# Kernel tuning notes

Measured on AMD Instinct MI355X. Metric: run time of the kernel, lower is better.

The kernel has to match this reference:

```python
import jax, jax.numpy as jnp
import numpy as np

L, B, E, H = 2048, 2, 1024, 16
HD = E // H


def setup_inputs() -> dict:
    key = jax.random.key(0)
    ks = jax.random.split(key, 5)
    s = 0.02
    return {
        "query": jax.random.normal(ks[0], (L, B, E), jnp.float32),
        "key": jax.random.normal(ks[1], (L, B, E), jnp.float32),
        "value": jax.random.normal(ks[2], (L, B, E), jnp.float32),
        "in_proj_weight": jax.random.normal(ks[3], (3 * E, E), jnp.float32) * s,
        "in_proj_bias": jnp.zeros((3 * E,), jnp.float32),
        "out_proj_weight": jax.random.normal(ks[4], (E, E), jnp.float32) * s,
        "out_proj_bias": jnp.zeros((E,), jnp.float32),
    }


def reference(query, key, value, in_proj_weight, in_proj_bias, out_proj_weight, out_proj_bias):
    # torch nn.MultiheadAttention math, seq-first [L, B, E], causal mask
    # (attend_mode='only_attend_front': positions j > i are masked).
    w_q, w_k, w_v = jnp.split(in_proj_weight, 3, axis=0)
    b_q, b_k, b_v = jnpp_split(in_proj_bias) if False else jnp.split(in_proj_bias, 3, axis=0)
    q = query @ w_q.T + b_q            # [L, B, E]
    k = key @ w_k.T + b_k
    v = value @ w_v.T + b_v

    def heads(x):  # [L, B, E] -> [B, H, L, HD]
        return x.reshape(x.shape[0], x.shape[1], H, HD).transpose(1, 2, 0, 3)

    qh, kh, vh = heads(q), heads(k), heads(v)
    scale = 1.0 / jnp.sqrt(jnp.asarray(HD, q.dtype))
    scores = jnp.einsum("bhqd,bhkd->bhqk", qh * scale, kh)  # [B, H, L, L]
    causal = jnp.triu(jnp.ones((scores.shape[-2], scores.shape[-1]), bool), k=1)
    scores = jnp.where(causal, jnp.asarray(-jnp.inf, scores.dtype), scores)
    attn = jax.nn.softmax(scores, axis=-1)
    out = jnp.einsum("bhqk,bhkd->bhqd", attn, vh)           # [B, H, L, HD]
    out = out.transpose(2, 0, 1, 3).reshape(query.shape[0], query.shape[1], E)  # [L, B, E]
    out = out @ out_proj_weight.T + out_proj_bias
    # torch also returns head-averaged attn weights [B, L, L]
    attn_avg = attn.mean(axis=1)
    return out, attn_avg
```

## Files before the change

### kernel.cpp

```cpp
#include <hip/hip_runtime.h>

#define L_ 2048
#define B_ 2
#define E_ 1024
#define H_ 16
#define HD_ 64
#define M_ 4096
#define K_ 1024

typedef unsigned short u16;
typedef unsigned int u32;
using short8  = __attribute__((ext_vector_type(8))) short;
using short4v = __attribute__((ext_vector_type(4))) short;
using floatx4 = __attribute__((ext_vector_type(4))) float;

__device__ inline u16 f2b(float f) {
  unsigned u = __float_as_uint(f);
  u += 0x7FFF + ((u >> 16) & 1);
  return (u16)(u >> 16);
}

__device__ inline u32 pack2(float a, float b) {
  u32 ua = __float_as_uint(a) + 0x8000u;
  u32 ub = __float_as_uint(b) + 0x8000u;
  return (ua >> 16) | (ub & 0xFFFF0000u);
}

__device__ inline floatx4 mfma16(short8 a, short8 b, floatx4 c) {
  return __builtin_amdgcn_mfma_f32_16x16x32_bf16(a, b, c, 0, 0, 0);
}

__device__ inline void gload16(const void* g, void* l) {
  __builtin_amdgcn_global_load_lds(
      (const __attribute__((address_space(1))) u32*)g,
      (__attribute__((address_space(3))) u32*)l, 16, 0, 0);
}

__global__ void convk(const float* __restrict__ src, u16* __restrict__ dst, int n4) {
  int i = blockIdx.x * blockDim.x + threadIdx.x;
  if (i < n4) {
    float4 v = ((const float4*)src)[i];
    ushort4 o;
    o.x = f2b(v.x); o.y = f2b(v.y); o.z = f2b(v.z); o.w = f2b(v.w);
    ((ushort4*)dst)[i] = o;
  }
}

template <int MODE>
__global__ __launch_bounds__(256) void gemm128(
    const u16* __restrict__ A, const u16* __restrict__ W, const float* __restrict__ bias,
    u16* __restrict__ qh, u16* __restrict__ kh, u16* __restrict__ vhT,
    float* __restrict__ outp)
{
  __shared__ __align__(16) u16 As[128 * 32];
  __shared__ __align__(16) u16 Bs[128 * 32];
  const int p = (MODE == 0) ? blockIdx.z : 0;
  const u16* Ap = A + (size_t)p * M_ * K_;
  const u16* Wp = W + (size_t)p * E_ * K_;
  const float* bp = bias + p * E_;
  const int row0 = blockIdx.y * 128, col0 = blockIdx.x * 128;
  const int t = threadIdx.x, lane = t & 63, wv = t >> 6;
  const int lanem = lane & 15, quad = lane >> 4;
  const int wm = wv >> 1, wn = wv & 1;

  int f0 = t, f1 = 256 + t;
  int r0s = f0 >> 2, q0s = (f0 & 3) ^ ((r0s >> 1) & 3);
  int r1s = f1 >> 2, q1s = (f1 & 3) ^ ((r1s >> 1) & 3);

  floatx4 acc[4][4];
#pragma unroll
  for (int mi = 0; mi < 4; ++mi)
#pragma unroll
    for (int ni = 0; ni < 4; ++ni) acc[mi][ni] = (floatx4){0.f, 0.f, 0.f, 0.f};

  const int swz = (lanem >> 1) & 3;

  for (int k0 = 0; k0 < K_; k0 += 32) {
    __syncthreads();
    gload16(Ap + (size_t)(row0 + r0s) * K_ + k0 + q0s * 8, (char*)As + wv * 1024);
    gload16(Wp + (size_t)(col0 + r0s) * K_ + k0 + q0s * 8, (char*)Bs + wv * 1024);
    gload16(Ap + (size_t)(row0 + r1s) * K_ + k0 + q1s * 8, (char*)As + 4096 + wv * 1024);
    gload16(Wp + (size_t)(col0 + r1s) * K_ + k0 + q1s * 8, (char*)Bs + 4096 + wv * 1024);
    __syncthreads();
    short8 af[4], bfg[4];
#pragma unroll
    for (int mi = 0; mi < 4; ++mi) {
      int r = wm * 64 + mi * 16 + lanem;
      af[mi] = *(const short8*)((const char*)As + r * 64 + (quad ^ swz) * 16);
    }
#pragma unroll
    for (int ni = 0; ni < 4; ++ni) {
      int r = wn * 64 + ni * 16 + lanem;
      bfg[ni] = *(const short8*)((const char*)Bs + r * 64 + (quad ^ swz) * 16);
    }
#pragma unroll
    for (int mi = 0; mi < 4; ++mi)
#pragma unroll
      for (int ni = 0; ni < 4; ++ni)
        acc[mi][ni] = mfma16(af[mi], bfg[ni], acc[mi][ni]);
  }

#pragma unroll
  for (int ni = 0; ni < 4; ++ni) {
    int gc = col0 + wn * 64 + ni * 16 + lanem;
    float bv = bp[gc];
#pragma unroll
    for (int mi = 0; mi < 4; ++mi) {
      int gr0 = row0 + wm * 64 + mi * 16 + quad * 4;
#pragma unroll
      for (int v = 0; v < 4; ++v) {
        float val = acc[mi][ni][v] + bv;
        int r = gr0 + v;
        if (MODE == 1) {
          outp[(size_t)r * E_ + gc] = val;
        } else {
          int l = r >> 1, bb = r & 1, hh = gc >> 6, d = gc & 63;
          u16 x = f2b(val);
          if (p == 0)      qh[(((size_t)bb * H_ + hh) * L_ + l) * HD_ + d] = x;
          else if (p == 1) kh[(((size_t)bb * H_ + hh) * L_ + l) * HD_ + d] = x;
          else {
            int lp = (l & ~31) | (((l >> 2) & 3) * 8 + ((l >> 4) & 1) * 4 + (l & 3));
            vhT[(((size_t)bb * H_ + hh) * HD_ + d) * L_ + lp] = x;
          }
        }
      }
    }
  }
}

__global__ __launch_bounds__(256, 2) void attn1(
    const u16* __restrict__ qh, const u16* __restrict__ kh, const u16* __restrict__ vhT,
    u16* __restrict__ ctx, float* __restrict__ li_ws)
{
  __shared__ __align__(16) u16 Ks[2][64 * 64];
  __shared__ __align__(16) u16 Vs[2][64 * 64];
  const int g = blockIdx.x;
  const int h = blockIdx.y, b = blockIdx.z;
  const int t = threadIdx.x, lane = t & 63, wv = t >> 6;
  const int lanem = lane & 15, quad = lane >> 4;
  const int bh = b * H_ + h;
  const int gB = (L_ / 64 - 1) - g;
  const int rowA = g * 64 + wv * 16 + lanem;
  const int rowB = gB * 64 + wv * 16 + lanem;

  const u16* qpA = qh + ((size_t)bh * L_ + rowA) * HD_;
  const u16* qpB = qh + ((size_t)bh * L_ + rowB) * HD_;
  short8 qA0 = *(const short8*)(qpA + quad * 8);
  short8 qA1 = *(const short8*)(qpA + 32 + quad * 8);
  short8 qB0 = *(const short8*)(qpB + quad * 8);
  short8 qB1 = *(const short8*)(qpB + 32 + quad * 8);

  const int srow = lane >> 3;
  const int spiece = (lane & 7) ^ srow;
  const u16* ksrc = kh + ((size_t)bh * L_ + wv * 16 + srow) * HD_ + spiece * 8;
  const u16* vsrc = vhT + ((size_t)bh * HD_ + wv * 16 + srow) * L_ + spiece * 8;

  const int ntiles = 32 - g;
  auto stage = [&](int buf) {
    gload16(ksrc, (char*)Ks[buf] + wv * 2048);
    gload16(ksrc + 8 * HD_, (char*)Ks[buf] + wv * 2048 + 1024);
    gload16(vsrc, (char*)Vs[buf] + wv * 2048);
    gload16(vsrc + (size_t)8 * L_, (char*)Vs[buf] + wv * 2048 + 1024);
    ksrc += 64 * HD_;
    vsrc += 64;
  };

  const int swz = lanem & 7;
  const int cb0 = lanem * 128 + ((quad ^ swz)) * 16;
  const int cb1 = lanem * 128 + ((quad ^ swz) ^ 4) * 16;

  float liA = 0.f, liB = 0.f;
  floatx4 oA[4], oB[4];
#pragma unroll
  for (int d = 0; d < 4; ++d) { oA[d] = (floatx4){0.f,0.f,0.f,0.f}; oB[d] = oA[d]; }

  int j0 = 0, tcur = 0;

  auto do_tile = [&](int modeA, int modeB) {
    __syncthreads();
    if (tcur + 1 < ntiles) stage((tcur + 1) & 1);
    const char* kbuf = (const char*)Ks[tcur & 1];
    const char* vbuf = (const char*)Vs[tcur & 1];

    floatx4 sA[4], sB[4];
#pragma unroll
    for (int jf = 0; jf < 4; ++jf) {
      short8 a0 = *(const short8*)(kbuf + cb0 + jf * 2048);
      short8 a1 = *(const short8*)(kbuf + cb1 + jf * 2048);
      floatx4 z = (floatx4){0.f,0.f,0.f,0.f};
      if (modeA != 2) sA[jf] = mfma16(a1, qA1, mfma16(a0, qA0, z));
      sB[jf] = mfma16(a1, qB1, mfma16(a0, qB0, z));
    }

    short8 pbA[2], pbB[2];
    auto soft = [&](floatx4* st, int row, float& li, short8* pb, int masked) {
#pragma unroll
      for (int jc = 0; jc < 2; ++jc) {
        float p[8];
#pragma unroll
        for (int r = 0; r < 4; ++r) {
          int ja = j0 + jc * 32 + quad * 4 + r;
          float e0 = __expf(st[jc * 2][r] * 0.125f);
          float e1 = __expf(st[jc * 2 + 1][r] * 0.125f);
          if (masked) {
            e0 = (ja <= row) ? e0 : 0.f;
            e1 = (ja + 16 <= row) ? e1 : 0.f;
          }
          li += e0 + e1;
          p[r] = e0; p[4 + r] = e1;
        }
        union { u32 w[4]; short8 s; } u;
        u.w[0] = pack2(p[0], p[1]); u.w[1] = pack2(p[2], p[3]);
        u.w[2] = pack2(p[4], p[5]); u.w[3] = pack2(p[6], p[7]);
        pb[jc] = u.s;
      }
    };
    if (modeA == 0) soft(sA, rowA, liA, pbA, 0);
    else if (modeA == 1) soft(sA, rowA, liA, pbA, 1);
    if (modeB == 0) soft(sB, rowB, liB, pbB, 0);
    else soft(sB, rowB, liB, pbB, 1);

#pragma unroll
    for (int jc = 0; jc < 2; ++jc) {
      const int base = (jc == 0) ? cb0 : cb1;
#pragma unroll
      for (int dbl = 0; dbl < 4; ++dbl) {
        short8 vf = *(const short8*)(vbuf + base + dbl * 2048);
        if (modeA != 2) oA[dbl] = mfma16(vf, pbA[jc], oA[dbl]);
        oB[dbl] = mfma16(vf, pbB[jc], oB[dbl]);
      }
    }
    j0 += 64;
    ++tcur;
  };

  stage(0);
  for (int jt = 0; jt < g; ++jt) do_tile(0, 0);
  do_tile(1, 0);
  for (int jt = g + 1; jt <= 30 - g; ++jt) do_tile(2, 0);
  do_tile(2, 1);

  liA += __shfl_xor(liA, 16); liA += __shfl_xor(liA, 32);
  liB += __shfl_xor(liB, 16); liB += __shfl_xor(liB, 32);
  float invA = 1.0f / liA, invB = 1.0f / liB;

  u16* cA = ctx + ((size_t)rowA * B_ + b) * E_ + h * HD_ + quad * 4;
  u16* cB = ctx + ((size_t)rowB * B_ + b) * E_ + h * HD_ + quad * 4;
#pragma unroll
  for (int dbl = 0; dbl < 4; ++dbl) {
    ushort4 pkA, pkB;
    pkA.x = f2b(oA[dbl][0] * invA); pkA.y = f2b(oA[dbl][1] * invA);
    pkA.z = f2b(oA[dbl][2] * invA); pkA.w = f2b(oA[dbl][3] * invA);
    pkB.x = f2b(oB[dbl][0] * invB); pkB.y = f2b(oB[dbl][1] * invB);
    pkB.z = f2b(oB[dbl][2] * invB); pkB.w = f2b(oB[dbl][3] * invB);
    *(ushort4*)(cA + dbl * 16) = pkA;
    *(ushort4*)(cB + dbl * 16) = pkB;
  }
  if (quad == 0) {
    li_ws[(size_t)bh * L_ + rowA] = invA;
    li_ws[(size_t)bh * L_ + rowB] = invB;
  }
}

__global__ __launch_bounds__(256) void attn2(
    const u16* __restrict__ qh, const u16* __restrict__ kh,
    const float* __restrict__ li_ws, float* __restrict__ out2)
{
  __shared__ __align__(16) u16 Ks[2][2][64 * 64];
  const int jt = blockIdx.x, it = blockIdx.y, b = blockIdx.z;
  const int t = threadIdx.x, lane = t & 63, wv = t >> 6;
  const int lanem = lane & 15, quad = lane >> 4;
  const int i0 = it * 64 + wv * 16;
  const int j0 = jt * 64;
  float* ob = out2 + (size_t)b * L_ * L_;

  if (jt > it) {
    float4 z = {0.f, 0.f, 0.f, 0.f};
    float* rp = ob + (size_t)(i0 + lanem) * L_ + j0 + quad * 16;
    ((float4*)rp)[0] = z; ((float4*)rp)[1] = z;
    ((float4*)rp)[2] = z; ((float4*)rp)[3] = z;
    return;
  }

  const int srow = lane >> 3;
  const int spiece = (lane & 7) ^ srow;
  const int swz = lanem & 7;

  auto stage = [&](int p, int buf) {
#pragma unroll
    for (int hh = 0; hh < 2; ++hh) {
      const u16* kg = kh + ((size_t)(b * H_ + 2 * p + hh) * L_ + j0) * HD_;
#pragma unroll
      for (int k = wv * 2; k < wv * 2 + 2; ++k)
        gload16(kg + (size_t)(k * 8 + srow) * HD_ + spiece * 8,
                (char*)Ks[buf][hh] + k * 1024);
    }
  };
  auto loadQ = [&](int p, short8 q[2][2], floatx4 lf[2]) {
#pragma unroll
    for (int hh = 0; hh < 2; ++hh) {
      int bh = b * H_ + 2 * p + hh;
      const u16* qb = qh + ((size_t)bh * L_ + i0 + lanem) * HD_;
      q[hh][0] = *(const short8*)(qb + quad * 8);
      q[hh][1] = *(const short8*)(qb + 32 + quad * 8);
      lf[hh] = *(const floatx4*)(li_ws + (size_t)bh * L_ + i0 + quad * 4);
    }
  };

  float acc[4][4] = {};
  short8 qc[2][2]; floatx4 lc[2];
  stage(0, 0);
  loadQ(0, qc, lc);

#pragma unroll
  for (int p = 0; p < 8; ++p) {
    const int buf = p & 1;
    __syncthreads();
    if (p < 7) stage(p + 1, 1 - buf);
    short8 qn[2][2]; floatx4 ln[2];
    loadQ(p < 7 ? p + 1 : 7, qn, ln);
#pragma unroll
    for (int hh = 0; hh < 2; ++hh) {
      const char* tb = (const char*)Ks[buf][hh];
#pragma unroll
      for (int s = 0; s < 4; ++s) {
        if (j0 + s * 16 > i0 + 15) continue;
        const char* kr = tb + (s * 16 + lanem) * 128;
        short8 b0 = *(const short8*)(kr + (quad ^ swz) * 16);
        short8 b1 = *(const short8*)(kr + ((4 + quad) ^ swz) * 16);
        floatx4 sv = (floatx4){0.f, 0.f, 0.f, 0.f};
        sv = mfma16(qc[hh][0], b0, sv);
        sv = mfma16(qc[hh][1], b1, sv);
        if (j0 + s * 16 + 15 <= i0) {
#pragma unroll
          for (int r = 0; r < 4; ++r)
            acc[s][r] += __expf(sv[r] * 0.125f) * lc[hh][r];
        } else {
#pragma unroll
          for (int r = 0; r < 4; ++r) {
            int irow = i0 + quad * 4 + r;
            int jc = j0 + s * 16 + lanem;
            if (jc <= irow) acc[s][r] += __expf(sv[r] * 0.125f) * lc[hh][r];
          }
        }
      }
    }
#pragma unroll
    for (int hh = 0; hh < 2; ++hh) {
      qc[hh][0] = qn[hh][0]; qc[hh][1] = qn[hh][1]; lc[hh] = ln[hh];
    }
  }

#pragma unroll
  for (int s = 0; s < 4; ++s)
#pragma unroll
    for (int r = 0; r < 4; ++r) {
      int irow = i0 + quad * 4 + r;
      int jc = j0 + s * 16 + lanem;
      ob[(size_t)irow * L_ + jc] = acc[s][r] * (1.0f / H_);
    }
}

extern "C" void kernel_launch(void* const* d_in, const int* in_sizes, int n_in,
                              void* d_out, int out_size, void* d_ws, size_t ws_size,
                              hipStream_t stream) {
  const float* query = (const float*)d_in[0];
  const float* key   = (const float*)d_in[1];
  const float* value = (const float*)d_in[2];
  const float* w_in  = (const float*)d_in[3];
  const float* b_in  = (const float*)d_in[4];
  const float* w_out = (const float*)d_in[5];
  const float* b_out = (const float*)d_in[6];

  char* ws = (char*)d_ws;
  size_t off = 0;
  auto alloc = [&](size_t bytes) -> void* {
    void* p = ws + off;
    off += (bytes + 255) & ~(size_t)255;
    return p;
  };
  u16* w_in_b  = (u16*)alloc((size_t)3 * E_ * K_ * 2);
  u16* w_out_b = (u16*)alloc((size_t)E_ * K_ * 2);
  u16* x_b     = (u16*)alloc((size_t)3 * M_ * K_ * 2);
  u16* qh      = (u16*)alloc((size_t)B_ * H_ * L_ * HD_ * 2);
  u16* kh      = (u16*)alloc((size_t)B_ * H_ * L_ * HD_ * 2);
  u16* vhT     = (u16*)alloc((size_t)B_ * H_ * L_ * HD_ * 2);
  u16* ctx     = (u16*)alloc((size_t)M_ * E_ * 2);
  float* li_ws = (float*)alloc((size_t)B_ * H_ * L_ * 4);

  convk<<<4096, 256, 0, stream>>>(query, x_b + (size_t)0 * M_ * K_, M_ * K_ / 4);
  convk<<<4096, 256, 0, stream>>>(key,   x_b + (size_t)1 * M_ * K_, M_ * K_ / 4);
  convk<<<4096, 256, 0, stream>>>(value, x_b + (size_t)2 * M_ * K_, M_ * K_ / 4);
  convk<<<3072, 256, 0, stream>>>(w_in,  w_in_b,  3 * E_ * K_ / 4);
  convk<<<1024, 256, 0, stream>>>(w_out, w_out_b, E_ * K_ / 4);

  gemm128<0><<<dim3(E_ / 128, M_ / 128, 3), 256, 0, stream>>>(
      x_b, w_in_b, b_in, qh, kh, vhT, nullptr);

  attn1<<<dim3(L_ / 128, H_, B_), 256, 0, stream>>>(qh, kh, vhT, ctx, li_ws);

  attn2<<<dim3(L_ / 64, L_ / 64, B_), 256, 0, stream>>>(
      qh, kh, li_ws, (float*)d_out + (size_t)M_ * E_);

  gemm128<1><<<dim3(E_ / 128, M_ / 128, 1), 256, 0, stream>>>(
      ctx, w_out_b, b_out, nullptr, nullptr, nullptr, (float*)d_out);
}
```

Measured before the change: 274.3 us.

## Double-buffer GEMM LDS tiles and merge conversion launches into one kernel

The GEMM kernel now uses two LDS buffers and issues the global-to-LDS load for the next K slice before computing on the current one. This removes one barrier per iteration and aims to overlap memory latency with MFMA work. The five separate fp32-to-bf16 conversion launches are merged into a single launch indexed by blockIdx.z, which cuts launch overhead. The cost is doubled LDS use per block, which may lower occupancy, and the overlap depends on how the compiler places its memory-count waits.

```diff
diff --git a/kernel.cpp b/kernel.cpp
--- a/kernel.cpp
+++ b/kernel.cpp
@@ -36,12 +36,24 @@
       (__attribute__((address_space(3))) u32*)l, 16, 0, 0);
 }
 
-__global__ void convk(const float* __restrict__ src, u16* __restrict__ dst, int n4) {
+__global__ void convall(const float* __restrict__ q, const float* __restrict__ k,
+                        const float* __restrict__ v, const float* __restrict__ wi,
+                        const float* __restrict__ wo,
+                        u16* __restrict__ xb, u16* __restrict__ wib,
+                        u16* __restrict__ wob) {
+  const int z = blockIdx.z;
+  const float* src;
+  u16* dst;
+  int n4;
+  if (z < 3)      { src = (z == 0 ? q : (z == 1 ? k : v));
+                    dst = xb + (size_t)z * M_ * K_; n4 = M_ * K_ / 4; }
+  else if (z == 3){ src = wi; dst = wib; n4 = 3 * E_ * K_ / 4; }
+  else            { src = wo; dst = wob; n4 = E_ * K_ / 4; }
   int i = blockIdx.x * blockDim.x + threadIdx.x;
   if (i < n4) {
-    float4 v = ((const float4*)src)[i];
+    float4 val = ((const float4*)src)[i];
     ushort4 o;
-    o.x = f2b(v.x); o.y = f2b(v.y); o.z = f2b(v.z); o.w = f2b(v.w);
+    o.x = f2b(val.x); o.y = f2b(val.y); o.z = f2b(val.z); o.w = f2b(val.w);
     ((ushort4*)dst)[i] = o;
   }
 }
@@ -52,8 +64,8 @@
     u16* __restrict__ qh, u16* __restrict__ kh, u16* __restrict__ vhT,
     float* __restrict__ outp)
 {
-  __shared__ __align__(16) u16 As[128 * 32];
-  __shared__ __align__(16) u16 Bs[128 * 32];
+  __shared__ __align__(16) u16 As[2][128 * 32];
+  __shared__ __align__(16) u16 Bs[2][128 * 32];
   const int p = (MODE == 0) ? blockIdx.z : 0;
   const u16* Ap = A + (size_t)p * M_ * K_;
   const u16* Wp = W + (size_t)p * E_ * K_;
@@ -75,23 +87,28 @@
 
   const int swz = (lanem >> 1) & 3;
 
+  auto STAGE = [&](int buf, int k0) {
+    gload16(Ap + (size_t)(row0 + r0s) * K_ + k0 + q0s * 8, (char*)As[buf] + wv * 1024);
+    gload16(Wp + (size_t)(col0 + r0s) * K_ + k0 + q0s * 8, (char*)Bs[buf] + wv * 1024);
+    gload16(Ap + (size_t)(row0 + r1s) * K_ + k0 + q1s * 8, (char*)As[buf] + 4096 + wv * 1024);
+    gload16(Wp + (size_t)(col0 + r1s) * K_ + k0 + q1s * 8, (char*)Bs[buf] + 4096 + wv * 1024);
+  };
+
+  STAGE(0, 0);
   for (int k0 = 0; k0 < K_; k0 += 32) {
+    const int buf = (k0 >> 5) & 1;
     __syncthreads();
-    gload16(Ap + (size_t)(row0 + r0s) * K_ + k0 + q0s * 8, (char*)As + wv * 1024);
-    gload16(Wp + (size_t)(col0 + r0s) * K_ + k0 + q0s * 8, (char*)Bs + wv * 1024);
-    gload16(Ap + (size_t)(row0 + r1s) * K_ + k0 + q1s * 8, (char*)As + 4096 + wv * 1024);
-    gload16(Wp + (size_t)(col0 + r1s) * K_ + k0 + q1s * 8, (char*)Bs + 4096 + wv * 1024);
-    __syncthreads();
+    if (k0 + 32 < K_) STAGE(buf ^ 1, k0 + 32);
     short8 af[4], bfg[4];
 #pragma unroll
     for (int mi = 0; mi < 4; ++mi) {
       int r = wm * 64 + mi * 16 + lanem;
-      af[mi] = *(const short8*)((const char*)As + r * 64 + (quad ^ swz) * 16);
+      af[mi] = *(const short8*)((const char*)As[buf] + r * 64 + (quad ^ swz) * 16);
     }
 #pragma unroll
     for (int ni = 0; ni < 4; ++ni) {
       int r = wn * 64 + ni * 16 + lanem;
-      bfg[ni] = *(const short8*)((const char*)Bs + r * 64 + (quad ^ swz) * 16);
+      bfg[ni] = *(const short8*)((const char*)Bs[buf] + r * 64 + (quad ^ swz) * 16);
     }
 #pragma unroll
     for (int mi = 0; mi < 4; ++mi)
@@ -388,11 +405,8 @@
   u16* ctx     = (u16*)alloc((size_t)M_ * E_ * 2);
   float* li_ws = (float*)alloc((size_t)B_ * H_ * L_ * 4);
 
-  convk<<<4096, 256, 0, stream>>>(query, x_b + (size_t)0 * M_ * K_, M_ * K_ / 4);
-  convk<<<4096, 256, 0, stream>>>(key,   x_b + (size_t)1 * M_ * K_, M_ * K_ / 4);
-  convk<<<4096, 256, 0, stream>>>(value, x_b + (size_t)2 * M_ * K_, M_ * K_ / 4);
-  convk<<<3072, 256, 0, stream>>>(w_in,  w_in_b,  3 * E_ * K_ / 4);
-  convk<<<1024, 256, 0, stream>>>(w_out, w_out_b, E_ * K_ / 4);
+  convall<<<dim3(4096, 1, 5), 256, 0, stream>>>(
+      query, key, value, w_in, w_out, x_b, w_in_b, w_out_b);
 
   gemm128<0><<<dim3(E_ / 128, M_ / 128, 3), 256, 0, stream>>>(
       x_b, w_in_b, b_in, qh, kh, vhT, nullptr);
```

Result: faster. 265.3 us (-3.3%).
